# Kernel tuning notes

Hardware: AMD Instinct MI355X
Metric: run time of the kernel (lower is better)

Reference implementation:

```python
import jax, jax.numpy as jnp
import numpy as np

B, S, D, H, HD, I = 8, 512, 2048, 32, 64, 8192
REL = 2 * 512 - 1  # 1023
EPS = 1e-6
SCALE = float(np.sqrt(HD))


def _layernorm(x, g, b):
    mu = jnp.mean(x, axis=-1, keepdims=True)
    var = jnp.mean(jnp.square(x - mu), axis=-1, keepdims=True)
    return (x - mu) / jnp.sqrt(var + EPS) * g + b


def setup_inputs() -> dict:
    key = jax.random.key(0)
    ks = jax.random.split(key, 10)
    s = 0.02
    return {
        "hidden_states": jax.random.normal(ks[0], (B, S, D), dtype=jnp.float32),
        "wq": jax.random.normal(ks[1], (D, D), dtype=jnp.float32) * s,
        "wk": jax.random.normal(ks[2], (D, D), dtype=jnp.float32) * s,
        "wv": jax.random.normal(ks[3], (D, D), dtype=jnp.float32) * s,
        "wo": jax.random.normal(ks[4], (D, D), dtype=jnp.float32) * s,
        "rel_pos": jax.random.normal(ks[5], (REL, HD), dtype=jnp.float32),
        "ln1_g": jnp.ones((D,), jnp.float32),
        "ln1_b": jnp.zeros((D,), jnp.float32),
        "gate_w": jax.random.normal(ks[6], (D, I), dtype=jnp.float32) * s,
        "up_w": jax.random.normal(ks[7], (D, I), dtype=jnp.float32) * s,
        "down_w": jax.random.normal(ks[8], (I, D), dtype=jnp.float32) * s,
        "ln2_g": jnp.ones((D,), jnp.float32),
        "ln2_b": jnp.zeros((D,), jnp.float32),
    }


def reference(hidden_states, wq, wk, wv, wo, rel_pos, ln1_g, ln1_b,
              gate_w, up_w, down_w, ln2_g, ln2_b):
    x = hidden_states
    # --- MultiHeadAttentionXL ---
    q = (x @ wq).reshape(B, S, H, HD)
    k = (x @ wk).reshape(B, S, H, HD)
    v = (x @ wv).reshape(B, S, H, HD)
    scores = jnp.einsum('bqhd,bkhd->bhqk', q, k) / SCALE
    # relative position bias (seq_len <= 512 path)
    pos = jnp.arange(S)
    rp = jnp.clip(pos[None, :] - pos[:, None] + 512 - 1, 0, REL - 1)  # [S,S]
    bias = rel_pos[rp].mean(axis=-1)  # [S,S]
    scores = scores + bias[None, None]
    attn = jax.nn.softmax(scores, axis=-1)
    ctx = jnp.einsum('bhqk,bkhd->bqhd', attn, v).reshape(B, S, D)
    attn_out = ctx @ wo
    # residual + post-LN
    h = _layernorm(x + attn_out, ln1_g, ln1_b)
    # --- FeedForwardXL (SwiGLU) ---
    gate = jax.nn.silu(h @ gate_w)
    up = h @ up_w
    ffn = (gate * up) @ down_w
    h = _layernorm(h + ffn, ln2_g, ln2_b)
    return h
```

## Files before the change

kernel.cpp:

```cpp
#include <hip/hip_runtime.h>
#include <cstdint>
#include <cstddef>

typedef _Float16 f16;
typedef _Float16 f16x8 __attribute__((ext_vector_type(8)));
typedef _Float16 f16x4 __attribute__((ext_vector_type(4)));
typedef float    f32x4 __attribute__((ext_vector_type(4)));

constexpr int S_ = 512, D_ = 2048, H_ = 32, HD_ = 64, I_ = 8192;
constexpr int M_ = 4096;
constexpr int IH_ = 4096;

enum { OP_F32 = 0, OP_QKT = 3, OP_PV = 4, OP_QKV = 6, OP_GU = 9, OP_ADD = 10 };

__device__ __forceinline__ void gl_lds16(const void* g, void* lds) {
  __builtin_amdgcn_global_load_lds(
      (const __attribute__((address_space(1))) void*)g,
      (__attribute__((address_space(3))) void*)lds, 16, 0, 0);
}

template <int BM, int BN, int WR, int WC, int OP, int BK>
__global__ __launch_bounds__(256, 2) void gemm_k(
    const f16* __restrict__ A, int lda,
    const f16* __restrict__ B, int ldb,
    void* __restrict__ Cp, int ldc,
    int K, int bh0, const float* __restrict__ relmean,
    const f16* __restrict__ B2) {
  static_assert(WR * WC == 4, "4-wave blocks assumed");
  static_assert(BK == 32 || BK == 64, "");
  constexpr bool GU = (OP == OP_GU);
  constexpr int WM = BM / WR, WN = BN / WC;
  constexpr int IM = WM / 16, IN = WN / 16;
  constexpr int RR = (BK == 64) ? 8 : 16;
  constexpr int CA = BM * BK / 2048;
  constexpr int CB = BN * BK / 2048;
  constexpr int KS = BK / 32;
  __shared__ __align__(16) f16 As[BM * BK];
  __shared__ __align__(16) f16 Bs[(GU ? 2 : 1) * BN * BK];
  const int tid = threadIdx.x, wave = tid >> 6, lane = tid & 63;
  const int wm = wave / WC, wn = wave % WC;
  const int bn = blockIdx.x, bm = blockIdx.y, bz = blockIdx.z;

  long aoff = 0, boff = 0;
  if constexpr (OP == OP_QKT) {
    int bh = bh0 + bz;
    long hb = (long)(bh >> 5) * (S_ * D_) + (long)(bh & (H_ - 1)) * HD_;
    aoff = hb; boff = hb;
  }
  if constexpr (OP == OP_PV) {
    int bh = bh0 + bz;
    aoff = (long)bz * S_ * S_;
    boff = (long)bh * HD_ * S_;
  }
  if constexpr (OP == OP_QKV) boff = (long)bz * D_ * D_;

  const f16* Ab = A + aoff + (long)bm * BM * lda;
  const f16* Bb = B + boff + (long)bn * BN * ldb;
  const f16* Bb2 = nullptr;
  if constexpr (GU) Bb2 = B2 + (long)bn * BN * ldb;

  f32x4 acc[IM][IN], acc2[GU ? IM : 1][GU ? IN : 1];
#pragma unroll
  for (int i = 0; i < IM; i++)
#pragma unroll
    for (int j = 0; j < IN; j++) {
      acc[i][j] = {0.f, 0.f, 0.f, 0.f};
      if constexpr (GU) acc2[i][j] = {0.f, 0.f, 0.f, 0.f};
    }

  const int lrr = (BK == 64) ? (lane >> 3) : (lane >> 2);
  const int lcc = (BK == 64) ? (lane & 7) : (lane & 3);
  const int scc = (BK == 64) ? (lcc ^ (lrr & 7)) : lcc;
  const int g = lane >> 4, l15 = lane & 15;

  for (int kt = 0; kt < K; kt += BK) {
    if (kt) __syncthreads();
#pragma unroll
    for (int c = 0; c < CA; c++) {
      int reg = wave * CA + c;
      gl_lds16(Ab + (long)(reg * RR + lrr) * lda + kt + scc * 8, &As[reg * 512]);
    }
#pragma unroll
    for (int c = 0; c < CB; c++) {
      int reg = wave * CB + c;
      gl_lds16(Bb + (long)(reg * RR + lrr) * ldb + kt + scc * 8, &Bs[reg * 512]);
      if constexpr (GU)
        gl_lds16(Bb2 + (long)(reg * RR + lrr) * ldb + kt + scc * 8,
                 &Bs[BN * BK + reg * 512]);
    }
    __syncthreads();
    f16x8 af[KS][IM], bf[KS][IN], bf2[GU ? KS : 1][GU ? IN : 1];
#pragma unroll
    for (int s = 0; s < KS; s++) {
#pragma unroll
      for (int i = 0; i < IM; i++) {
        int row = wm * WM + i * 16 + l15;
        int cidx = s * 4 + g;
        if constexpr (BK == 64) cidx ^= (row & 7);
        af[s][i] = *(const f16x8*)&As[row * BK + cidx * 8];
      }
#pragma unroll
      for (int j = 0; j < IN; j++) {
        int colL = wn * WN + j * 16 + l15;
        int cidx = s * 4 + g;
        if constexpr (BK == 64) cidx ^= (colL & 7);
        bf[s][j] = *(const f16x8*)&Bs[colL * BK + cidx * 8];
        if constexpr (GU) bf2[s][j] = *(const f16x8*)&Bs[BN * BK + colL * BK + cidx * 8];
      }
    }
#pragma unroll
    for (int s = 0; s < KS; s++)
#pragma unroll
      for (int i = 0; i < IM; i++)
#pragma unroll
        for (int j = 0; j < IN; j++) {
          acc[i][j] = __builtin_amdgcn_mfma_f32_16x16x32_f16(af[s][i], bf[s][j], acc[i][j], 0, 0, 0);
          if constexpr (GU)
            acc2[i][j] = __builtin_amdgcn_mfma_f32_16x16x32_f16(af[s][i], bf2[s][j], acc2[i][j], 0, 0, 0);
        }
  }

  const int r0 = bm * BM + wm * WM + (lane >> 4) * 4;
  const int c0 = bn * BN + wn * WN + l15;
#pragma unroll
  for (int i = 0; i < IM; i++) {
#pragma unroll
    for (int j = 0; j < IN; j++) {
      int rowb = r0 + i * 16;
      int col = c0 + j * 16;
      if constexpr (OP == OP_F32) {
        float* C = (float*)Cp;
#pragma unroll
        for (int t = 0; t < 4; t++) C[(long)(rowb + t) * ldc + col] = acc[i][j][t];
      } else if constexpr (OP == OP_ADD) {
        float* C = (float*)Cp;
#pragma unroll
        for (int t = 0; t < 4; t++) C[(long)(rowb + t) * ldc + col] += acc[i][j][t];
      } else if constexpr (OP == OP_GU) {
        f16* C = (f16*)Cp;
#pragma unroll
        for (int t = 0; t < 4; t++) {
          float gg = acc[i][j][t], u = acc2[i][j][t];
          C[(long)(rowb + t) * ldc + col] = (f16)(gg / (1.f + __expf(-gg)) * u);
        }
      } else if constexpr (OP == OP_QKT) {
        f16* C = (f16*)Cp + (long)bz * S_ * S_;
#pragma unroll
        for (int t = 0; t < 4; t++) {
          int r = rowb + t;
          C[(long)r * S_ + col] = (f16)(acc[i][j][t] * 0.125f + relmean[col - r + 511]);
        }
      } else if constexpr (OP == OP_PV) {
        int bh = bh0 + bz;
        f16* C = (f16*)Cp + (long)(bh >> 5) * (S_ * D_) + (long)(bh & (H_ - 1)) * HD_;
#pragma unroll
        for (int t = 0; t < 4; t++) C[(long)(rowb + t) * ldc + col] = (f16)acc[i][j][t];
      } else if constexpr (OP == OP_QKV) {
        f16* C = (f16*)Cp;
        if (bz < 2) {
          f16* Cq = C + (long)bz * M_ * D_;
#pragma unroll
          for (int t = 0; t < 4; t++) Cq[(long)(rowb + t) * ldc + col] = (f16)acc[i][j][t];
        } else {
          f16* Cv = C + (long)2 * M_ * D_;
          int b = rowb >> 9, s0 = rowb & 511, h = col >> 6, hd = col & 63;
          f16x4 pk;
#pragma unroll
          for (int t = 0; t < 4; t++) pk[t] = (f16)acc[i][j][t];
          *(f16x4*)&Cv[((long)(b * H_ + h) * HD_ + hd) * S_ + s0] = pk;
        }
      }
    }
  }
}

__global__ __launch_bounds__(256) void transpose_k(
    const float* __restrict__ in, int ldin, int k0, int n0,
    f16* __restrict__ out, int ldout) {
  __shared__ f16 t[64][68];
  const int kb = blockIdx.x * 64, nb = blockIdx.y * 64;
  const int tid = threadIdx.x;
  {
    const int kr = tid >> 4, nc = (tid & 15) * 4;
    const float* src = in + (long)(k0 + kb) * ldin + (n0 + nb);
#pragma unroll
    for (int i = 0; i < 4; i++) {
      int k = kr + i * 16;
      f32x4 v = *(const f32x4*)&src[(long)k * ldin + nc];
#pragma unroll
      for (int j = 0; j < 4; j++) t[nc + j][k] = (f16)v[j];
    }
  }
  __syncthreads();
  {
    const int n = tid >> 2, kc = (tid & 3) * 16;
    f16* dst = out + (long)(nb + n) * ldout + (kb + kc);
#pragma unroll
    for (int j = 0; j < 4; j++)
      *(f16x4*)&dst[j * 4] = *(const f16x4*)&t[n][kc + j * 4];
  }
}

__global__ void cvt_f16_k(const float* __restrict__ in, f16* __restrict__ out, int n4) {
  int i = blockIdx.x * 256 + threadIdx.x;
  if (i >= n4) return;
  f32x4 v = ((const f32x4*)in)[i];
  f16x4 o;
#pragma unroll
  for (int t = 0; t < 4; t++) o[t] = (f16)v[t];
  ((f16x4*)out)[i] = o;
}

__global__ void relmean_k(const float* __restrict__ rel, float* __restrict__ rm) {
  int i = blockIdx.x * 256 + threadIdx.x;
  if (i >= 1023) return;
  float s = 0.f;
#pragma unroll 8
  for (int d = 0; d < 64; d++) s += rel[i * 64 + d];
  rm[i] = s * (1.f / 64.f);
}

__global__ __launch_bounds__(256) void softmax_k(f16* __restrict__ Sc) {
  int r = blockIdx.x * 4 + (threadIdx.x >> 6);
  int lane = threadIdx.x & 63;
  f16* s = Sc + (long)r * S_;
  f16x8 d = *(const f16x8*)&s[lane * 8];
  float v[8], mx = -1e30f;
#pragma unroll
  for (int i = 0; i < 8; i++) { v[i] = (float)d[i]; mx = fmaxf(mx, v[i]); }
  for (int off = 32; off; off >>= 1) mx = fmaxf(mx, __shfl_xor(mx, off));
  float sum = 0.f;
#pragma unroll
  for (int i = 0; i < 8; i++) { v[i] = __expf(v[i] - mx); sum += v[i]; }
  for (int off = 32; off; off >>= 1) sum += __shfl_xor(sum, off);
  float rs = 1.f / sum;
  f16x8 o;
#pragma unroll
  for (int i = 0; i < 8; i++) o[i] = (f16)(v[i] * rs);
  *(f16x8*)&s[lane * 8] = o;
}

__global__ __launch_bounds__(256) void ln1_k(const float* __restrict__ X,
                                             const float* __restrict__ Y,
                                             const float* __restrict__ g,
                                             const float* __restrict__ b,
                                             f16* __restrict__ outH) {
  int row = blockIdx.x;
  const float* x = X + (long)row * D_;
  const float* y = Y + (long)row * D_;
  int t = threadIdx.x;
  float v[8], sum = 0.f, sq = 0.f;
#pragma unroll
  for (int i = 0; i < 8; i++) {
    int idx = t + i * 256;
    float val = x[idx] + y[idx];
    v[i] = val; sum += val; sq += val * val;
  }
  for (int off = 32; off; off >>= 1) { sum += __shfl_down(sum, off); sq += __shfl_down(sq, off); }
  __shared__ float s1[4], s2[4];
  if ((t & 63) == 0) { s1[t >> 6] = sum; s2[t >> 6] = sq; }
  __syncthreads();
  sum = s1[0] + s1[1] + s1[2] + s1[3];
  sq = s2[0] + s2[1] + s2[2] + s2[3];
  float mu = sum * (1.f / D_);
  float rstd = rsqrtf(sq * (1.f / D_) - mu * mu + 1e-6f);
#pragma unroll
  for (int i = 0; i < 8; i++) {
    int idx = t + i * 256;
    outH[(long)row * D_ + idx] = (f16)((v[i] - mu) * rstd * g[idx] + b[idx]);
  }
}

__global__ __launch_bounds__(256) void ln2f_k(const float* __restrict__ X,
                                              const f16* __restrict__ Y,
                                              const float* __restrict__ g,
                                              const float* __restrict__ b,
                                              float* __restrict__ outF) {
  int row = blockIdx.x;
  const float* x = X + (long)row * D_;
  const f16* y = Y + (long)row * D_;
  int t = threadIdx.x;
  float v[8], sum = 0.f, sq = 0.f;
#pragma unroll
  for (int i = 0; i < 8; i++) {
    int idx = t + i * 256;
    float val = x[idx] + (float)y[idx];
    v[i] = val; sum += val; sq += val * val;
  }
  for (int off = 32; off; off >>= 1) { sum += __shfl_down(sum, off); sq += __shfl_down(sq, off); }
  __shared__ float s1[4], s2[4];
  if ((t & 63) == 0) { s1[t >> 6] = sum; s2[t >> 6] = sq; }
  __syncthreads();
  sum = s1[0] + s1[1] + s1[2] + s1[3];
  sq = s2[0] + s2[1] + s2[2] + s2[3];
  float mu = sum * (1.f / D_);
  float rstd = rsqrtf(sq * (1.f / D_) - mu * mu + 1e-6f);
#pragma unroll
  for (int i = 0; i < 8; i++) {
    int idx = t + i * 256;
    outF[(long)row * D_ + idx] = (v[i] - mu) * rstd * g[idx] + b[idx];
  }
}

extern "C" void kernel_launch(void* const* d_in, const int* in_sizes, int n_in,
                              void* d_out, int out_size, void* d_ws, size_t ws_size,
                              hipStream_t stream) {
  const float* x    = (const float*)d_in[0];
  const float* wq   = (const float*)d_in[1];
  const float* wk   = (const float*)d_in[2];
  const float* wv   = (const float*)d_in[3];
  const float* wo   = (const float*)d_in[4];
  const float* rel  = (const float*)d_in[5];
  const float* ln1g = (const float*)d_in[6];
  const float* ln1b = (const float*)d_in[7];
  const float* gw   = (const float*)d_in[8];
  const float* uw   = (const float*)d_in[9];
  const float* dw   = (const float*)d_in[10];
  const float* ln2g = (const float*)d_in[11];
  const float* ln2b = (const float*)d_in[12];
  float* out = (float*)d_out;

  constexpr size_t MD2 = (size_t)M_ * D_ * 2;
  if (ws_size < 8 * MD2 + 4096) return;
  char* w = (char*)d_ws;
  f16* qb   = (f16*)(w + 0 * MD2);
  f16* vT   = (f16*)(w + 2 * MD2);
  f16* xb   = (f16*)(w + 3 * MD2);
  f16* sc   = (f16*)(w + 4 * MD2);
  f16* h1h  = (f16*)(w + 6 * MD2);
  f16* s7   = (f16*)(w + 7 * MD2);
  float* relmean = (float*)(w + 8 * MD2);
  f16* ctxb = xb;
  float* attn_out = (float*)qb;
  f16* wqT  = sc;
  f16* woT  = s7;
  f16* gwTh = qb;
  f16* uwTh = (f16*)(w + 1 * MD2);
  f16* gch  = vT;
  f16* dwTh = s7;
  float* facc = (float*)sc;

  cvt_f16_k<<<M_ * D_ / 4 / 256, 256, 0, stream>>>(x, xb, M_ * D_ / 4);
  relmean_k<<<4, 256, 0, stream>>>(rel, relmean);
  transpose_k<<<dim3(32, 32), 256, 0, stream>>>(wq, D_, 0, 0, wqT, D_);
  transpose_k<<<dim3(32, 32), 256, 0, stream>>>(wk, D_, 0, 0, wqT + (size_t)D_ * D_, D_);
  transpose_k<<<dim3(32, 32), 256, 0, stream>>>(wv, D_, 0, 0, wqT + 2 * (size_t)D_ * D_, D_);
  transpose_k<<<dim3(32, 32), 256, 0, stream>>>(wo, D_, 0, 0, woT, D_);

  gemm_k<128, 128, 2, 2, OP_QKV, 32><<<dim3(16, 32, 3), 256, 0, stream>>>(
      xb, D_, wqT, D_, qb, D_, D_, 0, nullptr, nullptr);

  for (int c = 0; c < 4; c++) {
    int bh0 = c * 64;
    gemm_k<128, 128, 2, 2, OP_QKT, 64><<<dim3(4, 4, 64), 256, 0, stream>>>(
        qb, D_, qb + (size_t)M_ * D_, D_, sc, S_, HD_, bh0, relmean, nullptr);
    softmax_k<<<64 * S_ / 4, 256, 0, stream>>>(sc);
    gemm_k<64, 64, 2, 2, OP_PV, 64><<<dim3(1, 8, 64), 256, 0, stream>>>(
        sc, S_, vT, S_, ctxb, D_, S_, bh0, nullptr, nullptr);
  }

  gemm_k<128, 128, 2, 2, OP_F32, 32><<<dim3(16, 32, 1), 256, 0, stream>>>(
      ctxb, D_, woT, D_, attn_out, D_, D_, 0, nullptr, nullptr);
  ln1_k<<<M_, 256, 0, stream>>>(x, attn_out, ln1g, ln1b, h1h);

  for (int h = 0; h < 2; h++) {
    transpose_k<<<dim3(32, 64), 256, 0, stream>>>(gw, I_, 0, h * IH_, gwTh, D_);
    transpose_k<<<dim3(32, 64), 256, 0, stream>>>(uw, I_, 0, h * IH_, uwTh, D_);
    transpose_k<<<dim3(64, 32), 256, 0, stream>>>(dw, D_, h * IH_, 0, dwTh, IH_);
    gemm_k<128, 128, 2, 2, OP_GU, 32><<<dim3(IH_ / 128, 32, 1), 256, 0, stream>>>(
        h1h, D_, gwTh, D_, gch, IH_, D_, 0, nullptr, uwTh);
    if (h == 0)
      gemm_k<128, 128, 2, 2, OP_F32, 32><<<dim3(16, 32, 1), 256, 0, stream>>>(
          gch, IH_, dwTh, IH_, facc, D_, IH_, 0, nullptr, nullptr);
    else
      gemm_k<128, 128, 2, 2, OP_ADD, 32><<<dim3(16, 32, 1), 256, 0, stream>>>(
          gch, IH_, dwTh, IH_, facc, D_, IH_, 0, nullptr, nullptr);
  }
  ln2f_k<<<M_, 256, 0, stream>>>(facc, h1h, ln2g, ln2b, out);
}
```

Before: 1.165 ms.

## Fuse QK^T, relative bias, softmax and PV into a single attention kernel

Replaces the chunked pipeline of a QK^T GEMM, a standalone softmax kernel and a PV GEMM with one fused attention kernel. Each block loads one head's K and V into LDS and keeps its 16x512 score rows in registers per wave. It applies scale and relative-position bias and runs softmax in registers, then stages P through LDS for the PV MFMAs. This removes the round trips of the full fp16 score matrix through global memory and cuts the launch count. In exchange the kernel needs about 132KB of LDS per block and many accumulator registers, which limits occupancy.

```diff
diff --git a/kernel.cpp b/kernel.cpp
--- a/kernel.cpp
+++ b/kernel.cpp
@@ -174,6 +174,129 @@
   }
 }
 
+__global__ __launch_bounds__(512, 2) void fattn_k(
+    const f16* __restrict__ Q, const f16* __restrict__ Kg,
+    const f16* __restrict__ Vt, f16* __restrict__ Ctx,
+    const float* __restrict__ rel) {
+  __shared__ __align__(16) f16 Ks[512 * 64];
+  __shared__ __align__(16) f16 Vs[64 * 512];
+  __shared__ float rms[1024];
+  const int tid = threadIdx.x, wave = tid >> 6, lane = tid & 63;
+  const int g = lane >> 4, l15 = lane & 15;
+  const int lrr = lane >> 3, lcc = lane & 7;
+  const int bm = blockIdx.x, bh = blockIdx.y;
+  const int b = bh >> 5, h = bh & 31;
+  const long qrow0 = (long)b * S_ + bm * 128;
+  const long krow0 = (long)b * S_;
+  const int hoff = h * HD_;
+
+#pragma unroll
+  for (int c = 0; c < 8; c++) {
+    int reg = wave * 8 + c;
+    gl_lds16(Kg + (krow0 + reg * 8 + lrr) * D_ + hoff + (lcc ^ lrr) * 8,
+             &Ks[reg * 512]);
+  }
+  const f16* vb = Vt + (long)bh * HD_ * S_;
+#pragma unroll
+  for (int c = 0; c < 8; c++) {
+    int reg = wave * 8 + c;
+    int rb = reg >> 3, cb = reg & 7;
+    gl_lds16(vb + (long)(rb * 8 + lrr) * S_ + cb * 64 + (lcc ^ lrr) * 8,
+             &Vs[reg * 512]);
+  }
+  for (int i = tid; i < 1023; i += 512) rms[i] = rel[i];
+
+  f16x8 aq[2];
+#pragma unroll
+  for (int ks = 0; ks < 2; ks++)
+    aq[ks] = *(const f16x8*)&Q[(qrow0 + wave * 16 + l15) * D_ + hoff + ks * 32 + g * 8];
+
+  __syncthreads();
+
+  f32x4 acc[32];
+#pragma unroll
+  for (int jn = 0; jn < 32; jn++) acc[jn] = {0.f, 0.f, 0.f, 0.f};
+#pragma unroll
+  for (int jn = 0; jn < 32; jn++) {
+    int r = jn * 16 + l15;
+    f16x8 b0 = *(const f16x8*)&Ks[r * 64 + ((g) ^ (r & 7)) * 8];
+    f16x8 b1 = *(const f16x8*)&Ks[r * 64 + ((4 + g) ^ (r & 7)) * 8];
+    acc[jn] = __builtin_amdgcn_mfma_f32_16x16x32_f16(aq[0], b0, acc[jn], 0, 0, 0);
+    acc[jn] = __builtin_amdgcn_mfma_f32_16x16x32_f16(aq[1], b1, acc[jn], 0, 0, 0);
+  }
+
+  const int qr0 = bm * 128 + wave * 16 + g * 4;
+  float mx[4] = {-1e30f, -1e30f, -1e30f, -1e30f}, sum[4] = {0.f, 0.f, 0.f, 0.f};
+#pragma unroll
+  for (int t = 0; t < 4; t++) {
+    int bb = l15 - (qr0 + t) + 511;
+#pragma unroll
+    for (int jn = 0; jn < 32; jn++) {
+      float v = acc[jn][t] * 0.125f + rms[bb + jn * 16];
+      acc[jn][t] = v;
+      mx[t] = fmaxf(mx[t], v);
+    }
+  }
+#pragma unroll
+  for (int off = 8; off; off >>= 1)
+#pragma unroll
+    for (int t = 0; t < 4; t++) mx[t] = fmaxf(mx[t], __shfl_xor(mx[t], off));
+#pragma unroll
+  for (int t = 0; t < 4; t++)
+#pragma unroll
+    for (int jn = 0; jn < 32; jn++) {
+      float e = __expf(acc[jn][t] - mx[t]);
+      acc[jn][t] = e;
+      sum[t] += e;
+    }
+#pragma unroll
+  for (int off = 8; off; off >>= 1)
+#pragma unroll
+    for (int t = 0; t < 4; t++) sum[t] += __shfl_xor(sum[t], off);
+  float rs[4];
+#pragma unroll
+  for (int t = 0; t < 4; t++) rs[t] = 1.f / sum[t];
+
+  __syncthreads();
+
+  f16* Pb = &Ks[wave * 4096];
+  f32x4 aco[4];
+#pragma unroll
+  for (int jv = 0; jv < 4; jv++) aco[jv] = {0.f, 0.f, 0.f, 0.f};
+#pragma unroll
+  for (int hh = 0; hh < 2; hh++) {
+#pragma unroll
+    for (int jl = 0; jl < 16; jl++) {
+      int jn = hh * 16 + jl;
+      f16x4 w;
+#pragma unroll
+      for (int t = 0; t < 4; t++) w[t] = (f16)(acc[jn][t] * rs[t]);
+      *(f16x4*)&Pb[(jl * 16 + l15) * 16 + g * 4] = w;
+    }
+#pragma unroll
+    for (int kl = 0; kl < 8; kl++) {
+      f16x8 ap;
+#pragma unroll
+      for (int i = 0; i < 8; i++)
+        ap[i] = Pb[(kl * 32 + g * 8 + i) * 16 + l15];
+#pragma unroll
+      for (int jv = 0; jv < 4; jv++) {
+        int r = jv * 16 + l15, c = (hh * 8 + kl) * 4 + g;
+        f16x8 bv = *(const f16x8*)&Vs[(r >> 3) * 4096 + (c >> 3) * 512 +
+                                      (r & 7) * 64 + ((c & 7) ^ (r & 7)) * 8];
+        aco[jv] = __builtin_amdgcn_mfma_f32_16x16x32_f16(ap, bv, aco[jv], 0, 0, 0);
+      }
+    }
+  }
+
+#pragma unroll
+  for (int jv = 0; jv < 4; jv++)
+#pragma unroll
+    for (int t = 0; t < 4; t++)
+      Ctx[(qrow0 + wave * 16 + g * 4 + t) * D_ + hoff + jv * 16 + l15] =
+          (f16)aco[jv][t];
+}
+
 __global__ __launch_bounds__(256) void transpose_k(
     const float* __restrict__ in, int ldin, int k0, int n0,
     f16* __restrict__ out, int ldout) {
@@ -218,26 +341,6 @@
 #pragma unroll 8
   for (int d = 0; d < 64; d++) s += rel[i * 64 + d];
   rm[i] = s * (1.f / 64.f);
-}
-
-__global__ __launch_bounds__(256) void softmax_k(f16* __restrict__ Sc) {
-  int r = blockIdx.x * 4 + (threadIdx.x >> 6);
-  int lane = threadIdx.x & 63;
-  f16* s = Sc + (long)r * S_;
-  f16x8 d = *(const f16x8*)&s[lane * 8];
-  float v[8], mx = -1e30f;
-#pragma unroll
-  for (int i = 0; i < 8; i++) { v[i] = (float)d[i]; mx = fmaxf(mx, v[i]); }
-  for (int off = 32; off; off >>= 1) mx = fmaxf(mx, __shfl_xor(mx, off));
-  float sum = 0.f;
-#pragma unroll
-  for (int i = 0; i < 8; i++) { v[i] = __expf(v[i] - mx); sum += v[i]; }
-  for (int off = 32; off; off >>= 1) sum += __shfl_xor(sum, off);
-  float rs = 1.f / sum;
-  f16x8 o;
-#pragma unroll
-  for (int i = 0; i < 8; i++) o[i] = (f16)(v[i] * rs);
-  *(f16x8*)&s[lane * 8] = o;
 }
 
 __global__ __launch_bounds__(256) void ln1_k(const float* __restrict__ X,
@@ -326,19 +429,19 @@
   f16* qb   = (f16*)(w + 0 * MD2);
   f16* vT   = (f16*)(w + 2 * MD2);
   f16* xb   = (f16*)(w + 3 * MD2);
-  f16* sc   = (f16*)(w + 4 * MD2);
+  f16* s45  = (f16*)(w + 4 * MD2);
   f16* h1h  = (f16*)(w + 6 * MD2);
   f16* s7   = (f16*)(w + 7 * MD2);
   float* relmean = (float*)(w + 8 * MD2);
   f16* ctxb = xb;
   float* attn_out = (float*)qb;
-  f16* wqT  = sc;
+  f16* wqT  = s45;
   f16* woT  = s7;
   f16* gwTh = qb;
   f16* uwTh = (f16*)(w + 1 * MD2);
   f16* gch  = vT;
   f16* dwTh = s7;
-  float* facc = (float*)sc;
+  float* facc = (float*)s45;
 
   cvt_f16_k<<<M_ * D_ / 4 / 256, 256, 0, stream>>>(x, xb, M_ * D_ / 4);
   relmean_k<<<4, 256, 0, stream>>>(rel, relmean);
@@ -350,14 +453,8 @@
   gemm_k<128, 128, 2, 2, OP_QKV, 32><<<dim3(16, 32, 3), 256, 0, stream>>>(
       xb, D_, wqT, D_, qb, D_, D_, 0, nullptr, nullptr);
 
-  for (int c = 0; c < 4; c++) {
-    int bh0 = c * 64;
-    gemm_k<128, 128, 2, 2, OP_QKT, 64><<<dim3(4, 4, 64), 256, 0, stream>>>(
-        qb, D_, qb + (size_t)M_ * D_, D_, sc, S_, HD_, bh0, relmean, nullptr);
-    softmax_k<<<64 * S_ / 4, 256, 0, stream>>>(sc);
-    gemm_k<64, 64, 2, 2, OP_PV, 64><<<dim3(1, 8, 64), 256, 0, stream>>>(
-        sc, S_, vT, S_, ctxb, D_, S_, bh0, nullptr, nullptr);
-  }
+  fattn_k<<<dim3(4, 256), 512, 0, stream>>>(
+      qb, qb + (size_t)M_ * D_, vT, ctxb, relmean);
 
   gemm_k<128, 128, 2, 2, OP_F32, 32><<<dim3(16, 32, 1), 256, 0, stream>>>(
       ctxb, D_, woT, D_, attn_out, D_, D_, 0, nullptr, nullptr);
```

Result: faster. 1.086 ms (-6.7%).
